# Kernel optimization log

Measured on AMD Instinct MI355X. Metric: run time of the kernel, lower is better.

Reference implementation:

```python
import jax, jax.numpy as jnp
import numpy as np

N, E = 50000, 500000
A, R, EB, EH, H, C, AH, SH, S, AV = 64, 20, 32, 64, 4, 32, 128, 64, 32, 32
EPS = 1e-8
MAX_DIST = 0.5   # nm, maximum_interaction_radius
SCALE = 1.0      # nm, scale_factor


def physnet_rbf(d):
    # PhysNet radial basis: exp(-beta * (exp(-d) - mu_k)^2), mu_k in [exp(-r_cut), 1]
    mu = jnp.linspace(np.exp(-MAX_DIST), 1.0, R).astype(jnp.float32)
    beta = jnp.float32((2.0 / R * (1.0 - np.exp(-MAX_DIST))) ** -2)
    return jnp.exp(-beta * (jnp.exp(-d)[:, None] - mu) ** 2)  # [E, R]


def _forward(h, x, v, idx_i, idx_j, W_edge_in, b_edge_in, W_edge_h, b_edge_h,
             W_edge_out, b_edge_out, W_att, b_att, W_x_mix, W_node1, b_node1,
             W_node2, b_node2, W_post1, b_post1, W_post2, b_post2,
             W_vel1, b_vel1, W_vel2, w_v_mix):
    n = h.shape[0]
    act = jax.nn.silu
    seg_sum = lambda t, idx: jax.ops.segment_sum(t, idx, num_segments=n)

    # geometry
    r_ij = x[idx_j] - x[idx_i]                       # [E,3]
    d_ij = jnp.sqrt(jnp.sum(r_ij * r_ij, -1) + EPS)  # [E]
    dir_ij = r_ij / (d_ij[:, None] + EPS)            # [E,3]

    # update_edge: gather, RBF filter, edge MLP
    h_cat = jnp.concatenate([h[idx_i], h[idx_j]], -1)                 # [E,2A]
    filtered = physnet_rbf(d_ij) * (h_cat @ W_edge_in + b_edge_in)    # [E,R]
    e_in = jnp.concatenate([h_cat, filtered, d_ij[:, None] / SCALE], -1)
    h_ij_edge = act(e_in @ W_edge_h + b_edge_h) @ W_edge_out + b_edge_out  # [E,EB]

    # semantic attention: CELU logits + segment softmax over receivers per head
    logits = jax.nn.celu(h_ij_edge @ W_att + b_att, alpha=2.0)        # [E,H]
    seg_max = jax.ops.segment_max(logits, idx_i, num_segments=n)      # [n,H]
    exp_l = jnp.exp(logits - seg_max[idx_i])
    denom = seg_sum(exp_l, idx_i)
    att = exp_l / (denom[idx_i] + EPS)                                # [E,H]
    h_ij_semantic = (att[:, :, None] * h_ij_edge[:, None, :]).reshape(-1, H * EB)

    # neighborhood aggregation (scatter-add)
    h_i_semantic = seg_sum(h_ij_semantic, idx_i)                      # [n,H*EB]

    # spatial attention
    mix = jnp.tanh(h_ij_semantic @ W_x_mix)                           # [E,C]
    combinations = dir_ij[:, None, :] * mix[:, :, None]               # [E,C,3]
    counts = jnp.maximum(seg_sum(jnp.ones((idx_i.shape[0],), h.dtype), idx_i), 1.0)
    comb_mean = seg_sum(combinations, idx_i) / counts[:, None, None]  # scatter-mean
    comb_norm2 = jnp.sum(comb_mean * comb_mean, -1)                   # [n,C]
    h_i_spatial = act(act(comb_norm2 @ W_post1 + b_post1) @ W_post2 + b_post2)

    # node update (residual)
    node_in = jnp.concatenate([h, h_i_semantic, h_i_spatial], -1)
    h_upd = h + act(act(node_in @ W_node1 + b_node1) @ W_node2 + b_node2)

    # velocity / coordinate update
    v_ij = jnp.einsum('ecx,c->ex', combinations, w_v_mix)             # [E,3]
    dv = seg_sum(v_ij, idx_i) / counts[:, None]                       # scatter-mean
    gate = 2.0 * jax.nn.sigmoid(act(h_upd @ W_vel1 + b_vel1) @ W_vel2)  # [n,1]
    v_upd = gate * v + dv
    x_upd = x + v_upd
    return h_upd, x_upd, v_upd


def _p(k, shape, scale=0.05):
    return jax.random.normal(k, shape, dtype=jnp.float32) * scale


def setup_inputs() -> dict:
    key = jax.random.key(0)
    ks = jax.random.split(key, 24)
    return {
        'h': jax.random.normal(ks[0], (N, A), dtype=jnp.float32),
        'x': jax.random.normal(ks[1], (N, 3), dtype=jnp.float32),
        'v': jax.random.normal(ks[2], (N, 3), dtype=jnp.float32),
        'idx_i': jax.random.randint(ks[3], (E,), 0, N),
        'idx_j': jax.random.randint(ks[4], (E,), 0, N),
        'W_edge_in': _p(ks[5], (2 * A, R)), 'b_edge_in': jnp.zeros((R,), jnp.float32),
        'W_edge_h': _p(ks[6], (2 * A + R + 1, EH)), 'b_edge_h': jnp.zeros((EH,), jnp.float32),
        'W_edge_out': _p(ks[7], (EH, EB)), 'b_edge_out': jnp.zeros((EB,), jnp.float32),
        'W_att': _p(ks[8], (EB, H)), 'b_att': jnp.zeros((H,), jnp.float32),
        'W_x_mix': _p(ks[9], (H * EB, C)),
        'W_node1': _p(ks[10], (A + H * EB + S, AH)), 'b_node1': jnp.zeros((AH,), jnp.float32),
        'W_node2': _p(ks[11], (AH, A)), 'b_node2': jnp.zeros((A,), jnp.float32),
        'W_post1': _p(ks[12], (C, SH)), 'b_post1': jnp.zeros((SH,), jnp.float32),
        'W_post2': _p(ks[13], (SH, S)), 'b_post2': jnp.zeros((S,), jnp.float32),
        'W_vel1': _p(ks[14], (A, AV)), 'b_vel1': jnp.zeros((AV,), jnp.float32),
        'W_vel2': _p(ks[15], (AV, 1)),
        'w_v_mix': _p(ks[16], (C,)),
    }


def reference(h, x, v, idx_i, idx_j, W_edge_in, b_edge_in, W_edge_h, b_edge_h,
              W_edge_out, b_edge_out, W_att, b_att, W_x_mix, W_node1, b_node1,
              W_node2, b_node2, W_post1, b_post1, W_post2, b_post2,
              W_vel1, b_vel1, W_vel2, w_v_mix):
    return _forward(h, x, v, idx_i, idx_j, W_edge_in, b_edge_in, W_edge_h, b_edge_h,
                    W_edge_out, b_edge_out, W_att, b_att, W_x_mix, W_node1, b_node1,
                    W_node2, b_node2, W_post1, b_post1, W_post2, b_post2,
                    W_vel1, b_vel1, W_vel2, w_v_mix)
```

## Files before the change

kernel.cpp:

```cpp
#include <hip/hip_runtime.h>
#include <math.h>

#define DA 64
#define NODEIN_DIM 224
#define EPSC 1e-8f

typedef short v8s __attribute__((ext_vector_type(8)));
typedef float v4f __attribute__((ext_vector_type(4)));
typedef unsigned short ushort_t;

__device__ __forceinline__ float siluf(float v) { return v / (1.0f + __expf(-v)); }

__device__ __forceinline__ void atomAddF(float* p, float v) {
#if defined(__HIP_DEVICE_COMPILE__)
  unsafeAtomicAdd(p, v);
#else
  atomicAdd(p, v);
#endif
}

__device__ __forceinline__ unsigned short f2bfu(float f) {
  union { float f; unsigned u; } v; v.f = f;
  unsigned r = v.u + 0x7fffu + ((v.u >> 16) & 1u);
  return (unsigned short)(r >> 16);
}
__device__ __forceinline__ short f2bfs(float f) { return (short)f2bfu(f); }
__device__ __forceinline__ float bf2f(ushort_t s) {
  union { unsigned u; float f; } v; v.u = ((unsigned)s) << 16; return v.f;
}

#define MU0 0.60653065971263342f
#define DMU ((1.0f - 0.60653065971263342f) / 19.0f)
#define BETA ((float)(1.0 / (0.039346934028736658 * 0.039346934028736658)))

__global__ __launch_bounds__(256) void cast_h(
    const float* __restrict__ hsrc, ushort_t* __restrict__ hb, int n4)
{
  const int i = blockIdx.x * blockDim.x + threadIdx.x;
  if (i < n4) {
    const float4 fv = ((const float4*)hsrc)[i];
    ushort4 o;
    o.x = f2bfu(fv.x); o.y = f2bfu(fv.y); o.z = f2bfu(fv.z); o.w = f2bfu(fv.w);
    ((ushort4*)hb)[i] = o;
  }
}

__global__ __launch_bounds__(256) void deg_count(
    const int* __restrict__ idx_i, int* __restrict__ deg, int E)
{
  const int stride = gridDim.x * blockDim.x;
  for (int e = blockIdx.x * blockDim.x + threadIdx.x; e < E; e += stride)
    atomicAdd(&deg[idx_i[e]], 1);
}

#define SCAN_B 64
#define SCAN_T (SCAN_B * 256)

__global__ __launch_bounds__(256) void deg_tsum(
    const int* __restrict__ deg, int* __restrict__ tsum, int N, int C)
{
  const int g = blockIdx.x * blockDim.x + threadIdx.x;
  const int lo = g * C;
  const int hi = (lo + C < N) ? (lo + C) : N;
  int s = 0;
  for (int i = lo; i < hi; ++i) s += deg[i];
  tsum[g] = s;
}

__global__ __launch_bounds__(256) void scan_tsum(int* __restrict__ tsum)
{
  __shared__ int ps[256];
  const int t = threadIdx.x;
  const int per = SCAN_T / 256;
  const int lo = t * per;
  int s = 0;
  for (int i = 0; i < per; ++i) s += tsum[lo + i];
  ps[t] = s;
  __syncthreads();
  if (t == 0) {
    int a = 0;
    for (int i = 0; i < 256; ++i) { const int v = ps[i]; ps[i] = a; a += v; }
  }
  __syncthreads();
  int acc = ps[t];
  for (int i = 0; i < per; ++i) {
    const int v = tsum[lo + i];
    tsum[lo + i] = acc;
    acc += v;
  }
}

__global__ __launch_bounds__(256) void write_csr(
    const int* __restrict__ deg, const int* __restrict__ tpre,
    int* __restrict__ rowstart, int* __restrict__ cursor,
    float* __restrict__ counts, int N, int C)
{
  const int g = blockIdx.x * blockDim.x + threadIdx.x;
  const int lo = g * C;
  const int hi = (lo + C < N) ? (lo + C) : N;
  int acc = tpre[g];
  for (int i = lo; i < hi; ++i) {
    const int d = deg[i];
    rowstart[i] = acc;
    cursor[i] = acc;
    counts[i] = (float)d;
    acc += d;
  }
  if (hi == N) rowstart[N] = acc;
}

__global__ __launch_bounds__(256) void bucket_edges(
    const int* __restrict__ idx_i, const int* __restrict__ idx_j,
    int* __restrict__ cursor, int* __restrict__ iperm,
    int* __restrict__ jperm, int E)
{
  const int stride = gridDim.x * blockDim.x;
  for (int e = blockIdx.x * blockDim.x + threadIdx.x; e < E; e += stride) {
    const int ii = idx_i[e];
    const int pos = atomicAdd(&cursor[ii], 1);
    iperm[pos] = ii;
    jperm[pos] = idx_j[e];
  }
}

__global__ __launch_bounds__(256) void edge_f1(
    const ushort_t* __restrict__ h_bf, const float* __restrict__ x,
    const int* __restrict__ iperm, const int* __restrict__ jperm,
    const float* __restrict__ W_in, const float* __restrict__ b_in,
    ushort_t* __restrict__ Filt, float* __restrict__ dirb, int E)
{
  const int tid = blockIdx.x * blockDim.x + threadIdx.x;
  const int wid = tid >> 6;
  const int lane = threadIdx.x & 63;
  const int nw = (gridDim.x * blockDim.x) >> 6;
  const int l15 = lane & 15;
  const int q = lane >> 4;

  v8s bfr[4][2];
  #pragma unroll
  for (int kc = 0; kc < 4; ++kc)
    #pragma unroll
    for (int nt = 0; nt < 2; ++nt)
      #pragma unroll
      for (int j = 0; j < 8; ++j) {
        const int k = kc * 32 + q * 8 + j;
        const int col = nt * 16 + l15;
        bfr[kc][nt][j] = (col < 20) ? f2bfs(W_in[k * 20 + col]) : (short)0;
      }
  float bin[2], mu[2];
  #pragma unroll
  for (int nt = 0; nt < 2; ++nt) {
    const int col = nt * 16 + l15;
    bin[nt] = (col < 20) ? b_in[col] : 0.0f;
    mu[nt] = MU0 + (float)col * DMU;
  }

  const int ntiles = (E + 15) >> 4;
  for (int t = wid; t < ntiles; t += nw) {
    const int row = t * 16 + l15;
    const int rowL = (row < E) ? row : (E - 1);
    const int ii = iperm[rowL];
    const int jj = jperm[rowL];

    v8s afr[4];
    afr[0] = *(const v8s*)(h_bf + (size_t)ii * 64 + q * 8);
    afr[1] = *(const v8s*)(h_bf + (size_t)ii * 64 + 32 + q * 8);
    afr[2] = *(const v8s*)(h_bf + (size_t)jj * 64 + q * 8);
    afr[3] = *(const v8s*)(h_bf + (size_t)jj * 64 + 32 + q * 8);

    float dval = 0.0f;
    if (lane < 16 && row < E) {
      const float rx = x[jj * 3 + 0] - x[ii * 3 + 0];
      const float ry = x[jj * 3 + 1] - x[ii * 3 + 1];
      const float rz = x[jj * 3 + 2] - x[ii * 3 + 2];
      const float d = sqrtf(rx * rx + ry * ry + rz * rz + EPSC);
      dval = d;
      const float inv = 1.0f / (d + EPSC);
      dirb[row * 3 + 0] = rx * inv;
      dirb[row * 3 + 1] = ry * inv;
      dirb[row * 3 + 2] = rz * inv;
    }

    v4f acc[2];
    #pragma unroll
    for (int nt = 0; nt < 2; ++nt) {
      v4f a = {0.f, 0.f, 0.f, 0.f};
      #pragma unroll
      for (int kc = 0; kc < 4; ++kc)
        a = __builtin_amdgcn_mfma_f32_16x16x32_bf16(afr[kc], bfr[kc][nt], a, 0, 0, 0);
      acc[nt] = a;
    }

    const int rowb = t * 16 + q * 4;
    float dr[4], edr[4];
    #pragma unroll
    for (int r = 0; r < 4; ++r) {
      dr[r] = __shfl(dval, q * 4 + r);
      edr[r] = __expf(-dr[r]);
    }
    #pragma unroll
    for (int nt = 0; nt < 2; ++nt) {
      const int col = nt * 16 + l15;
      #pragma unroll
      for (int r = 0; r < 4; ++r) {
        ushort_t ov;
        if (col < 20) {
          const float tt = edr[r] - mu[nt];
          ov = f2bfu((acc[nt][r] + bin[nt]) * __expf(-BETA * tt * tt));
        } else if (col == 20) {
          ov = f2bfu(dr[r]);
        } else {
          ov = 0;
        }
        if (rowb + r < E) Filt[(size_t)(rowb + r) * 32 + col] = ov;
      }
    }
  }
}

#define THS 72
__global__ __launch_bounds__(256) void edge_f2(
    const ushort_t* __restrict__ h_bf,
    const int* __restrict__ iperm, const int* __restrict__ jperm,
    const ushort_t* __restrict__ Filt,
    const float* __restrict__ W_h, const float* __restrict__ b_h,
    const float* __restrict__ W_out, const float* __restrict__ b_out,
    const float* __restrict__ W_att, const float* __restrict__ b_att,
    ushort_t* __restrict__ heb, float* __restrict__ expl,
    float* __restrict__ denom, int E)
{
  __shared__ ushort_t sB2[20 * 64 * 8];
  __shared__ ushort_t sB3[4 * 64 * 8];
  __shared__ ushort_t tH[4][16 * THS];

  const int tid = threadIdx.x;
  for (int idx = tid; idx < 20 * 64 * 8; idx += 256) {
    const int j = idx & 7;
    const int ln = (idx >> 3) & 63;
    const int f = idx >> 9;
    const int k = (f >> 2) * 32 + (ln >> 4) * 8 + j;
    const int col = (f & 3) * 16 + (ln & 15);
    sB2[idx] = (k < 149) ? f2bfu(W_h[k * 64 + col]) : (ushort_t)0;
  }
  for (int idx = tid; idx < 4 * 64 * 8; idx += 256) {
    const int j = idx & 7;
    const int ln = (idx >> 3) & 63;
    const int f = idx >> 9;
    const int k = (f >> 1) * 32 + (ln >> 4) * 8 + j;
    const int col = (f & 1) * 16 + (ln & 15);
    sB3[idx] = f2bfu(W_out[k * 32 + col]);
  }
  __syncthreads();

  const int gtid = blockIdx.x * blockDim.x + tid;
  const int wid = gtid >> 6;
  const int lane = tid & 63;
  const int w = tid >> 6;
  const int nw = (gridDim.x * blockDim.x) >> 6;
  const int l15 = lane & 15;
  const int q = lane >> 4;

  const ushort_t* b2l = sB2 + lane * 8;
  const ushort_t* b3l = sB3 + lane * 8;

  float bias2[4];
  #pragma unroll
  for (int nt = 0; nt < 4; ++nt) bias2[nt] = b_h[nt * 16 + l15];
  float bias3[2];
  #pragma unroll
  for (int nt = 0; nt < 2; ++nt) bias3[nt] = b_out[nt * 16 + l15];

  v8s battf;
  #pragma unroll
  for (int j = 0; j < 8; ++j)
    battf[j] = (l15 < 4) ? f2bfs(W_att[(q * 8 + j) * 4 + l15]) : (short)0;
  const float bav = (l15 < 4) ? b_att[l15] : 0.0f;

  const int ntiles = (E + 15) >> 4;

  int iiC = 0;
  v8s afr[5];
  if (wid < ntiles) {
    const int row0 = wid * 16 + l15;
    const int rowL0 = (row0 < E) ? row0 : (E - 1);
    iiC = iperm[rowL0];
    const int jj0 = jperm[rowL0];
    afr[0] = *(const v8s*)(h_bf + (size_t)iiC * 64 + q * 8);
    afr[1] = *(const v8s*)(h_bf + (size_t)iiC * 64 + 32 + q * 8);
    afr[2] = *(const v8s*)(h_bf + (size_t)jj0 * 64 + q * 8);
    afr[3] = *(const v8s*)(h_bf + (size_t)jj0 * 64 + 32 + q * 8);
    afr[4] = *(const v8s*)(Filt + (size_t)rowL0 * 32 + q * 8);
  }

  for (int t = wid; t < ntiles; t += nw) {
    const int tn = t + nw;
    int iiN = 0;
    v8s nfr[5];
    if (tn < ntiles) {
      const int rowN = tn * 16 + l15;
      const int rowLN = (rowN < E) ? rowN : (E - 1);
      iiN = iperm[rowLN];
      const int jjN = jperm[rowLN];
      nfr[0] = *(const v8s*)(h_bf + (size_t)iiN * 64 + q * 8);
      nfr[1] = *(const v8s*)(h_bf + (size_t)iiN * 64 + 32 + q * 8);
      nfr[2] = *(const v8s*)(h_bf + (size_t)jjN * 64 + q * 8);
      nfr[3] = *(const v8s*)(h_bf + (size_t)jjN * 64 + 32 + q * 8);
      nfr[4] = *(const v8s*)(Filt + (size_t)rowLN * 32 + q * 8);
    }

    v4f acc2[4];
    #pragma unroll
    for (int nt = 0; nt < 4; ++nt) {
      v4f a = {0.f, 0.f, 0.f, 0.f};
      #pragma unroll
      for (int kc = 0; kc < 5; ++kc) {
        const v8s bfrag = *(const v8s*)(b2l + (kc * 4 + nt) * 512);
        a = __builtin_amdgcn_mfma_f32_16x16x32_bf16(afr[kc], bfrag, a, 0, 0, 0);
      }
      acc2[nt] = a;
    }

    #pragma unroll
    for (int nt = 0; nt < 4; ++nt) {
      #pragma unroll
      for (int r = 0; r < 4; ++r)
        tH[w][(q * 4 + r) * THS + nt * 16 + l15] =
            f2bfu(siluf(acc2[nt][r] + bias2[nt]));
    }
    __builtin_amdgcn_wave_barrier();

    v8s af3[2];
    af3[0] = *(const v8s*)&tH[w][l15 * THS + q * 8];
    af3[1] = *(const v8s*)&tH[w][l15 * THS + 32 + q * 8];

    v4f acc3[2];
    #pragma unroll
    for (int nt = 0; nt < 2; ++nt) {
      v4f a = {0.f, 0.f, 0.f, 0.f};
      #pragma unroll
      for (int kc = 0; kc < 2; ++kc) {
        const v8s bfrag = *(const v8s*)(b3l + (kc * 2 + nt) * 512);
        a = __builtin_amdgcn_mfma_f32_16x16x32_bf16(af3[kc], bfrag, a, 0, 0, 0);
      }
      acc3[nt] = a;
    }
    __builtin_amdgcn_wave_barrier();

    const int rowb = t * 16 + q * 4;
    #pragma unroll
    for (int nt = 0; nt < 2; ++nt) {
      const int col = nt * 16 + l15;
      #pragma unroll
      for (int r = 0; r < 4; ++r) {
        const ushort_t hv = f2bfu(acc3[nt][r] + bias3[nt]);
        tH[w][(q * 4 + r) * THS + col] = hv;
        if (rowb + r < E) heb[(size_t)(rowb + r) * 32 + col] = hv;
      }
    }
    __builtin_amdgcn_wave_barrier();

    const v8s afA = *(const v8s*)&tH[w][l15 * THS + q * 8];
    v4f az = {0.f, 0.f, 0.f, 0.f};
    const v4f aacc = __builtin_amdgcn_mfma_f32_16x16x32_bf16(afA, battf, az, 0, 0, 0);

    int ii_r[4];
    #pragma unroll
    for (int r = 0; r < 4; ++r) ii_r[r] = __shfl(iiC, q * 4 + r);

    if (l15 < 4) {
      #pragma unroll
      for (int r = 0; r < 4; ++r) {
        if (rowb + r < E) {
          const float la = aacc[r] + bav;
          const float l = (la > 0.f) ? la : 2.0f * (__expf(0.5f * la) - 1.0f);
          const float ev = __expf(l);
          expl[(size_t)(rowb + r) * 4 + l15] = ev;
          atomAddF(&denom[ii_r[r] * 4 + l15], ev);
        }
      }
    }
    __builtin_amdgcn_wave_barrier();

    iiC = iiN;
    afr[0] = nfr[0]; afr[1] = nfr[1]; afr[2] = nfr[2];
    afr[3] = nfr[3]; afr[4] = nfr[4];
  }
}

__global__ __launch_bounds__(256) void mix_kernel(
    const ushort_t* __restrict__ heb, const int* __restrict__ iperm,
    const float* __restrict__ expl, const float* __restrict__ denom,
    const float* __restrict__ W_xmix, const float* __restrict__ w_vmix,
    ushort_t* __restrict__ mixE, float* __restrict__ pE, int E)
{
  const int tid = blockIdx.x * blockDim.x + threadIdx.x;
  const int wid = tid >> 6;
  const int lane = threadIdx.x & 63;
  const int nw = (gridDim.x * blockDim.x) >> 6;
  const int l15 = lane & 15;
  const int q = lane >> 4;

  v8s bfr[4][2];
  #pragma unroll
  for (int kc = 0; kc < 4; ++kc)
    #pragma unroll
    for (int nt = 0; nt < 2; ++nt)
      #pragma unroll
      for (int j = 0; j < 8; ++j) {
        const int k = kc * 32 + q * 8 + j;
        const int col = nt * 16 + l15;
        bfr[kc][nt][j] = f2bfs(W_xmix[k * 32 + col]);
      }
  float wv[2];
  wv[0] = w_vmix[l15];
  wv[1] = w_vmix[16 + l15];

  const int ntiles = (E + 15) >> 4;
  for (int t = wid; t < ntiles; t += nw) {
    const int row = t * 16 + l15;
    const int rowL = (row < E) ? row : (E - 1);
    const int ii = iperm[rowL];
    float att[4];
    #pragma unroll
    for (int hh = 0; hh < 4; ++hh)
      att[hh] = expl[(size_t)rowL * 4 + hh] / (denom[ii * 4 + hh] + EPSC);

    const v8s hech = *(const v8s*)(heb + (size_t)rowL * 32 + q * 8);
    float hef[8];
    #pragma unroll
    for (int j = 0; j < 8; ++j) hef[j] = bf2f((ushort_t)hech[j]);

    v8s afr[4];
    #pragma unroll
    for (int kc = 0; kc < 4; ++kc)
      #pragma unroll
      for (int j = 0; j < 8; ++j)
        afr[kc][j] = f2bfs(att[kc] * hef[j]);

    v4f acc[2];
    #pragma unroll
    for (int nt = 0; nt < 2; ++nt) {
      v4f a = {0.f, 0.f, 0.f, 0.f};
      #pragma unroll
      for (int kc = 0; kc < 4; ++kc)
        a = __builtin_amdgcn_mfma_f32_16x16x32_bf16(afr[kc], bfr[kc][nt], a, 0, 0, 0);
      acc[nt] = a;
    }

    const int rowb = t * 16 + q * 4;
    float pr[4];
    #pragma unroll
    for (int r = 0; r < 4; ++r) {
      const float m0 = tanhf(acc[0][r]);
      const float m1 = tanhf(acc[1][r]);
      if (rowb + r < E) {
        mixE[(size_t)(rowb + r) * 32 + l15] = f2bfu(m0);
        mixE[(size_t)(rowb + r) * 32 + 16 + l15] = f2bfu(m1);
      }
      pr[r] = m0 * wv[0] + m1 * wv[1];
    }
    #pragma unroll
    for (int r = 0; r < 4; ++r) {
      pr[r] += __shfl_xor(pr[r], 1);
      pr[r] += __shfl_xor(pr[r], 2);
      pr[r] += __shfl_xor(pr[r], 4);
      pr[r] += __shfl_xor(pr[r], 8);
      if (l15 == 0 && rowb + r < E) pE[rowb + r] = pr[r];
    }
  }
}

__global__ __launch_bounds__(256) void node_reduce(
    const int* __restrict__ rowstart,
    const ushort_t* __restrict__ heb, const ushort_t* __restrict__ mixE,
    const float* __restrict__ expl, const float* __restrict__ denom,
    const float* __restrict__ dirb, const float* __restrict__ pE,
    ushort_t* __restrict__ hsem, float* __restrict__ comb_sum,
    float* __restrict__ dv_sum, int N)
{
  const int tid = blockIdx.x * blockDim.x + threadIdx.x;
  const int wid = tid >> 6;
  const int lane = threadIdx.x & 63;
  const int nw = (gridDim.x * blockDim.x) >> 6;
  const int hh = lane >> 5;
  const int eb = lane & 31;

  for (int n = wid; n < N; n += nw) {
    const int s = rowstart[n];
    const int epd = rowstart[n + 1];
    float semA = 0.f, semB = 0.f;
    float cx = 0.f, cy = 0.f, cz = 0.f;
    float dvx = 0.f, dvy = 0.f, dvz = 0.f;
    for (int k = s; k < epd; ++k) {
      const float he = bf2f(heb[(size_t)k * 32 + eb]);
      const float ea = expl[(size_t)k * 4 + hh];
      const float ec = expl[(size_t)k * 4 + 2 + hh];
      semA += ea * he;
      semB += ec * he;
      const float dx = dirb[k * 3 + 0];
      const float dy = dirb[k * 3 + 1];
      const float dz = dirb[k * 3 + 2];
      if (lane < 32) {
        const float m = bf2f(mixE[(size_t)k * 32 + lane]);
        cx += dx * m; cy += dy * m; cz += dz * m;
      }
      if (lane == 0) {
        const float pe = pE[k];
        dvx += dx * pe; dvy += dy * pe; dvz += dz * pe;
      }
    }
    const float dA = denom[n * 4 + hh] + EPSC;
    const float dB = denom[n * 4 + 2 + hh] + EPSC;
    hsem[(size_t)n * 128 + lane] = f2bfu(semA / dA);
    hsem[(size_t)n * 128 + 64 + lane] = f2bfu(semB / dB);
    if (lane < 32) {
      comb_sum[(size_t)n * 96 + lane * 3 + 0] = cx;
      comb_sum[(size_t)n * 96 + lane * 3 + 1] = cy;
      comb_sum[(size_t)n * 96 + lane * 3 + 2] = cz;
    }
    if (lane == 0) {
      dv_sum[n * 3 + 0] = dvx;
      dv_sum[n * 3 + 1] = dvy;
      dv_sum[n * 3 + 2] = dvz;
    }
  }
}

#define W1S 232
__global__ __launch_bounds__(256) void node_c1_mfma(
    const ushort_t* __restrict__ h_bf, const ushort_t* __restrict__ hsem,
    const float* __restrict__ comb_sum, const float* __restrict__ counts,
    const float* __restrict__ W_post1, const float* __restrict__ b_post1,
    const float* __restrict__ W_post2, const float* __restrict__ b_post2,
    const float* __restrict__ W_node1, const float* __restrict__ b_node1,
    ushort_t* __restrict__ nh_out, int N)
{
  __shared__ ushort_t sW1t[128 * W1S];
  __shared__ ushort_t tp[4][16 * THS];

  const int tid = threadIdx.x;
  for (int idx = tid; idx < 224 * 128; idx += 256) {
    const int k = idx >> 7;
    const int c = idx & 127;
    sW1t[c * W1S + k] = f2bfu(W_node1[idx]);
  }
  __syncthreads();

  const int lane = tid & 63;
  const int w = tid >> 6;
  const int l15 = lane & 15;
  const int q = lane >> 4;

  v8s bp1[4];
  #pragma unroll
  for (int nt = 0; nt < 4; ++nt)
    #pragma unroll
    for (int j = 0; j < 8; ++j)
      bp1[nt][j] = f2bfs(W_post1[(q * 8 + j) * 64 + nt * 16 + l15]);
  v8s bp2[2][2];
  #pragma unroll
  for (int kc = 0; kc < 2; ++kc)
    #pragma unroll
    for (int nt = 0; nt < 2; ++nt)
      #pragma unroll
      for (int j = 0; j < 8; ++j)
        bp2[kc][nt][j] = f2bfs(W_post2[(kc * 32 + q * 8 + j) * 32 + nt * 16 + l15]);
  float bb1[4];
  #pragma unroll
  for (int nt = 0; nt < 4; ++nt) bb1[nt] = b_post1[nt * 16 + l15];
  float bb2[2];
  #pragma unroll
  for (int nt = 0; nt < 2; ++nt) bb2[nt] = b_post2[nt * 16 + l15];
  float b1[8];
  #pragma unroll
  for (int nt = 0; nt < 8; ++nt) b1[nt] = b_node1[nt * 16 + l15];

  const int gw = blockIdx.x * 4 + w;
  const int nwv = gridDim.x * 4;
  const int ntiles = (N + 15) >> 4;

  for (int t = gw; t < ntiles; t += nwv) {
    const int row = t * 16 + l15;
    const int rowL = (row < N) ? row : (N - 1);

    const float inv = 1.0f / fmaxf(counts[rowL], 1.0f);
    const float4* cs = (const float4*)(comb_sum + (size_t)rowL * 96 + q * 24);
    float cf[24];
    #pragma unroll
    for (int b = 0; b < 6; ++b) {
      const float4 cv = cs[b];
      cf[b * 4 + 0] = cv.x; cf[b * 4 + 1] = cv.y;
      cf[b * 4 + 2] = cv.z; cf[b * 4 + 3] = cv.w;
    }
    v8s a1;
    #pragma unroll
    for (int j = 0; j < 8; ++j) {
      const float vx = cf[j * 3 + 0] * inv;
      const float vy = cf[j * 3 + 1] * inv;
      const float vz = cf[j * 3 + 2] * inv;
      a1[j] = f2bfs(vx * vx + vy * vy + vz * vz);
    }

    v4f p1[4];
    #pragma unroll
    for (int nt = 0; nt < 4; ++nt) {
      v4f a = {0.f, 0.f, 0.f, 0.f};
      p1[nt] = __builtin_amdgcn_mfma_f32_16x16x32_bf16(a1, bp1[nt], a, 0, 0, 0);
    }
    #pragma unroll
    for (int nt = 0; nt < 4; ++nt)
      #pragma unroll
      for (int r = 0; r < 4; ++r)
        tp[w][(q * 4 + r) * THS + nt * 16 + l15] =
            f2bfu(siluf(p1[nt][r] + bb1[nt]));
    __builtin_amdgcn_wave_barrier();

    v8s a2[2];
    a2[0] = *(const v8s*)&tp[w][l15 * THS + q * 8];
    a2[1] = *(const v8s*)&tp[w][l15 * THS + 32 + q * 8];

    v4f p2[2];
    #pragma unroll
    for (int nt = 0; nt < 2; ++nt) {
      v4f a = {0.f, 0.f, 0.f, 0.f};
      #pragma unroll
      for (int kc = 0; kc < 2; ++kc)
        a = __builtin_amdgcn_mfma_f32_16x16x32_bf16(a2[kc], bp2[kc][nt], a, 0, 0, 0);
      p2[nt] = a;
    }
    __builtin_amdgcn_wave_barrier();
    #pragma unroll
    for (int nt = 0; nt < 2; ++nt)
      #pragma unroll
      for (int r = 0; r < 4; ++r)
        tp[w][(q * 4 + r) * THS + nt * 16 + l15] =
            f2bfu(siluf(p2[nt][r] + bb2[nt]));
    __builtin_amdgcn_wave_barrier();

    v8s af[7];
    af[0] = *(const v8s*)(h_bf + (size_t)rowL * 64 + q * 8);
    af[1] = *(const v8s*)(h_bf + (size_t)rowL * 64 + 32 + q * 8);
    #pragma unroll
    for (int kc = 0; kc < 4; ++kc)
      af[2 + kc] = *(const v8s*)(hsem + (size_t)rowL * 128 + kc * 32 + q * 8);
    af[6] = *(const v8s*)&tp[w][l15 * THS + q * 8];

    v4f acc[8];
    #pragma unroll
    for (int nt = 0; nt < 8; ++nt) acc[nt] = (v4f){0.f, 0.f, 0.f, 0.f};
    #pragma unroll
    for (int kc = 0; kc < 7; ++kc) {
      #pragma unroll
      for (int nt = 0; nt < 8; ++nt) {
        const v8s bfrag =
            *(const v8s*)&sW1t[(nt * 16 + l15) * W1S + kc * 32 + q * 8];
        acc[nt] = __builtin_amdgcn_mfma_f32_16x16x32_bf16(af[kc], bfrag, acc[nt], 0, 0, 0);
      }
    }

    const int rowb = t * 16 + q * 4;
    #pragma unroll
    for (int nt = 0; nt < 8; ++nt) {
      #pragma unroll
      for (int r = 0; r < 4; ++r)
        if (rowb + r < N)
          nh_out[(size_t)(rowb + r) * 128 + nt * 16 + l15] =
              f2bfu(siluf(acc[nt][r] + b1[nt]));
    }
  }
}

__global__ __launch_bounds__(256) void node_c2_mfma(
    const float* __restrict__ h, const float* __restrict__ x,
    const float* __restrict__ v, const ushort_t* __restrict__ nh,
    const float* __restrict__ dv_sum, const float* __restrict__ counts,
    const float* __restrict__ W_node2, const float* __restrict__ b_node2,
    const float* __restrict__ W_vel1, const float* __restrict__ b_vel1,
    const float* __restrict__ W_vel2,
    float* __restrict__ out, int N)
{
  __shared__ ushort_t sW2[16 * 64 * 8];
  __shared__ ushort_t sWv[4 * 64 * 8];
  __shared__ ushort_t tH[4][16 * THS];
  __shared__ float sg[4][16];

  const int tid = threadIdx.x;
  for (int idx = tid; idx < 16 * 64 * 8; idx += 256) {
    const int j = idx & 7;
    const int ln = (idx >> 3) & 63;
    const int f = idx >> 9;
    const int k = (f >> 2) * 32 + (ln >> 4) * 8 + j;
    const int col = (f & 3) * 16 + (ln & 15);
    sW2[idx] = f2bfu(W_node2[k * 64 + col]);
  }
  for (int idx = tid; idx < 4 * 64 * 8; idx += 256) {
    const int j = idx & 7;
    const int ln = (idx >> 3) & 63;
    const int f = idx >> 9;
    const int k = (f >> 1) * 32 + (ln >> 4) * 8 + j;
    const int col = (f & 1) * 16 + (ln & 15);
    sWv[idx] = f2bfu(W_vel1[k * 32 + col]);
  }
  __syncthreads();

  const int lane = tid & 63;
  const int w = tid >> 6;
  const int l15 = lane & 15;
  const int q = lane >> 4;

  const ushort_t* w2l = sW2 + lane * 8;
  const ushort_t* wvl = sWv + lane * 8;

  float b2[4];
  #pragma unroll
  for (int nt = 0; nt < 4; ++nt) b2[nt] = b_node2[nt * 16 + l15];
  float bv[2];
  #pragma unroll
  for (int nt = 0; nt < 2; ++nt) bv[nt] = b_vel1[nt * 16 + l15];
  float wv2[2];
  #pragma unroll
  for (int nt = 0; nt < 2; ++nt) wv2[nt] = W_vel2[nt * 16 + l15];

  const int gw = blockIdx.x * 4 + w;
  const int nwv = gridDim.x * 4;
  const int ntiles = (N + 15) >> 4;

  for (int t = gw; t < ntiles; t += nwv) {
    const int row = t * 16 + l15;
    const int rowL = (row < N) ? row : (N - 1);

    v8s af[4];
    #pragma unroll
    for (int kc = 0; kc < 4; ++kc)
      af[kc] = *(const v8s*)(nh + (size_t)rowL * 128 + kc * 32 + q * 8);

    v4f acc[4];
    #pragma unroll
    for (int nt = 0; nt < 4; ++nt) {
      v4f a = {0.f, 0.f, 0.f, 0.f};
      #pragma unroll
      for (int kc = 0; kc < 4; ++kc) {
        const v8s bfrag = *(const v8s*)(w2l + (kc * 4 + nt) * 512);
        a = __builtin_amdgcn_mfma_f32_16x16x32_bf16(af[kc], bfrag, a, 0, 0, 0);
      }
      acc[nt] = a;
    }

    const int rowb = t * 16 + q * 4;
    #pragma unroll
    for (int nt = 0; nt < 4; ++nt) {
      const int col = nt * 16 + l15;
      #pragma unroll
      for (int r = 0; r < 4; ++r) {
        const int n = rowb + r;
        if (n < N) {
          const float hu = h[(size_t)n * 64 + col] + siluf(acc[nt][r] + b2[nt]);
          out[(size_t)n * 64 + col] = hu;
          tH[w][(q * 4 + r) * THS + col] = f2bfu(hu);
        }
      }
    }
    __builtin_amdgcn_wave_barrier();

    v8s a2[2];
    a2[0] = *(const v8s*)&tH[w][l15 * THS + q * 8];
    a2[1] = *(const v8s*)&tH[w][l15 * THS + 32 + q * 8];
    v4f av[2];
    #pragma unroll
    for (int nt = 0; nt < 2; ++nt) {
      v4f a = {0.f, 0.f, 0.f, 0.f};
      #pragma unroll
      for (int kc = 0; kc < 2; ++kc) {
        const v8s bfrag = *(const v8s*)(wvl + (kc * 2 + nt) * 512);
        a = __builtin_amdgcn_mfma_f32_16x16x32_bf16(a2[kc], bfrag, a, 0, 0, 0);
      }
      av[nt] = a;
    }

    #pragma unroll
    for (int r = 0; r < 4; ++r) {
      float pr = siluf(av[0][r] + bv[0]) * wv2[0] +
                 siluf(av[1][r] + bv[1]) * wv2[1];
      pr += __shfl_xor(pr, 1);
      pr += __shfl_xor(pr, 2);
      pr += __shfl_xor(pr, 4);
      pr += __shfl_xor(pr, 8);
      if (l15 == 0) sg[w][q * 4 + r] = 2.0f / (1.0f + __expf(-pr));
    }
    __builtin_amdgcn_wave_barrier();

    if (lane < 48) {
      const int rr = lane / 3;
      const int c = lane % 3;
      const int n = t * 16 + rr;
      if (n < N) {
        const float gate = sg[w][rr];
        const float cnt = fmaxf(counts[n], 1.0f);
        const float dv = dv_sum[n * 3 + c] / cnt;
        const float vu = gate * v[n * 3 + c] + dv;
        out[(size_t)N * 64 + (size_t)n * 3 + c] = x[n * 3 + c] + vu;
        out[(size_t)N * 64 + (size_t)N * 3 + (size_t)n * 3 + c] = vu;
      }
    }
    __builtin_amdgcn_wave_barrier();
  }
}

extern "C" void kernel_launch(void* const* d_in, const int* in_sizes, int n_in,
                              void* d_out, int out_size, void* d_ws, size_t ws_size,
                              hipStream_t stream) {
  const float* h   = (const float*)d_in[0];
  const float* x   = (const float*)d_in[1];
  const float* v   = (const float*)d_in[2];
  const int* idx_i = (const int*)d_in[3];
  const int* idx_j = (const int*)d_in[4];
  const float* W_edge_in  = (const float*)d_in[5];
  const float* b_edge_in  = (const float*)d_in[6];
  const float* W_edge_h   = (const float*)d_in[7];
  const float* b_edge_h   = (const float*)d_in[8];
  const float* W_edge_out = (const float*)d_in[9];
  const float* b_edge_out = (const float*)d_in[10];
  const float* W_att      = (const float*)d_in[11];
  const float* b_att      = (const float*)d_in[12];
  const float* W_x_mix    = (const float*)d_in[13];
  const float* W_node1    = (const float*)d_in[14];
  const float* b_node1    = (const float*)d_in[15];
  const float* W_node2    = (const float*)d_in[16];
  const float* b_node2    = (const float*)d_in[17];
  const float* W_post1    = (const float*)d_in[18];
  const float* b_post1    = (const float*)d_in[19];
  const float* W_post2    = (const float*)d_in[20];
  const float* b_post2    = (const float*)d_in[21];
  const float* W_vel1     = (const float*)d_in[22];
  const float* b_vel1     = (const float*)d_in[23];
  const float* W_vel2     = (const float*)d_in[24];
  const float* w_v_mix    = (const float*)d_in[25];

  const int E = in_sizes[3];
  const int N = in_sizes[0] / DA;

  float* ws = (float*)d_ws;
  size_t off = 0;
  float* denom    = ws + off; off += (size_t)N * 4;
  int*   deg      = (int*)(ws + off); off += (size_t)N;
  const size_t zeroBytes = off * sizeof(float);
  float* counts   = ws + off; off += (size_t)N;
  int*   rowstart = (int*)(ws + off); off += (size_t)N + 4;
  int*   cursor   = (int*)(ws + off); off += (size_t)N;
  int*   tsum     = (int*)(ws + off); off += (size_t)SCAN_T;
  int*   iperm    = (int*)(ws + off); off += (size_t)E;
  int*   jperm    = (int*)(ws + off); off += (size_t)E;
  float* pE       = ws + off; off += (size_t)E;
  float* expl     = ws + off; off += (size_t)E * 4;
  float* dirb     = ws + off; off += (size_t)E * 3;
  float* hsemR    = ws + off; off += (size_t)N * 64;
  float* comb_sum = ws + off; off += (size_t)N * 96;
  float* dv_sum   = ws + off; off += (size_t)N * 4;
  float* hbfR     = ws + off; off += (size_t)N * 32;
  float* fltR     = ws + off; off += (size_t)E * 16;
  float* hebR     = ws + off; off += (size_t)E * 16;

  ushort_t* h_bf = (ushort_t*)hbfR;
  ushort_t* hsem = (ushort_t*)hsemR;
  ushort_t* Filt = (ushort_t*)fltR;
  ushort_t* heb  = (ushort_t*)hebR;
  ushort_t* mixE = (ushort_t*)fltR;
  ushort_t* nh   = (ushort_t*)fltR;

  hipMemsetAsync(d_ws, 0, zeroBytes, stream);

  {
    const int n4 = (N * 64) / 4;
    cast_h<<<(n4 + 255) / 256, 256, 0, stream>>>(h, h_bf, n4);
  }
  deg_count<<<512, 256, 0, stream>>>(idx_i, deg, E);
  {
    const int C = (N + SCAN_T - 1) / SCAN_T;
    deg_tsum<<<SCAN_B, 256, 0, stream>>>(deg, tsum, N, C);
    scan_tsum<<<1, 256, 0, stream>>>(tsum);
    write_csr<<<SCAN_B, 256, 0, stream>>>(deg, tsum, rowstart, cursor, counts, N, C);
  }
  bucket_edges<<<512, 256, 0, stream>>>(idx_i, idx_j, cursor, iperm, jperm, E);
  edge_f1<<<1024, 256, 0, stream>>>(h_bf, x, iperm, jperm, W_edge_in,
                                    b_edge_in, Filt, dirb, E);
  edge_f2<<<1024, 256, 0, stream>>>(h_bf, iperm, jperm, Filt, W_edge_h,
                                    b_edge_h, W_edge_out, b_edge_out,
                                    W_att, b_att, heb, expl, denom, E);
  mix_kernel<<<1024, 256, 0, stream>>>(heb, iperm, expl, denom, W_x_mix,
                                       w_v_mix, mixE, pE, E);
  node_reduce<<<2048, 256, 0, stream>>>(rowstart, heb, mixE, expl, denom,
                                        dirb, pE, hsem, comb_sum, dv_sum, N);
  node_c1_mfma<<<512, 256, 0, stream>>>(
      h_bf, hsem, comb_sum, counts, W_post1, b_post1, W_post2, b_post2,
      W_node1, b_node1, nh, N);
  node_c2_mfma<<<512, 256, 0, stream>>>(
      h, x, v, nh, dv_sum, counts, W_node2, b_node2, W_vel1, b_vel1, W_vel2,
      (float*)d_out, N);
}
```

Baseline: 410.0 us.

## Fuse edge filter and edge MLP kernels, unroll node_reduce edge loop

Merges the RBF-filter kernel into the edge MLP kernel so the filtered features go through per-wave shared memory instead of a global Filt buffer, and reuses the gathered h fragments for both matmuls. This removes one kernel launch, the global write and re-read of Filt, and the duplicate gathers of h. The fused kernel uses more LDS (an extra W_in tile), which may lower occupancy. Separately, the per-node reduction loop is unrolled by four so more loads are in flight at once.

```diff
diff --git a/kernel.cpp b/kernel.cpp
--- a/kernel.cpp
+++ b/kernel.cpp
@@ -123,118 +123,32 @@
   }
 }
 
-__global__ __launch_bounds__(256) void edge_f1(
+#define THS 72
+__global__ __launch_bounds__(256) void edge_f12(
     const ushort_t* __restrict__ h_bf, const float* __restrict__ x,
     const int* __restrict__ iperm, const int* __restrict__ jperm,
     const float* __restrict__ W_in, const float* __restrict__ b_in,
-    ushort_t* __restrict__ Filt, float* __restrict__ dirb, int E)
-{
-  const int tid = blockIdx.x * blockDim.x + threadIdx.x;
-  const int wid = tid >> 6;
-  const int lane = threadIdx.x & 63;
-  const int nw = (gridDim.x * blockDim.x) >> 6;
-  const int l15 = lane & 15;
-  const int q = lane >> 4;
-
-  v8s bfr[4][2];
-  #pragma unroll
-  for (int kc = 0; kc < 4; ++kc)
-    #pragma unroll
-    for (int nt = 0; nt < 2; ++nt)
-      #pragma unroll
-      for (int j = 0; j < 8; ++j) {
-        const int k = kc * 32 + q * 8 + j;
-        const int col = nt * 16 + l15;
-        bfr[kc][nt][j] = (col < 20) ? f2bfs(W_in[k * 20 + col]) : (short)0;
-      }
-  float bin[2], mu[2];
-  #pragma unroll
-  for (int nt = 0; nt < 2; ++nt) {
-    const int col = nt * 16 + l15;
-    bin[nt] = (col < 20) ? b_in[col] : 0.0f;
-    mu[nt] = MU0 + (float)col * DMU;
-  }
-
-  const int ntiles = (E + 15) >> 4;
-  for (int t = wid; t < ntiles; t += nw) {
-    const int row = t * 16 + l15;
-    const int rowL = (row < E) ? row : (E - 1);
-    const int ii = iperm[rowL];
-    const int jj = jperm[rowL];
-
-    v8s afr[4];
-    afr[0] = *(const v8s*)(h_bf + (size_t)ii * 64 + q * 8);
-    afr[1] = *(const v8s*)(h_bf + (size_t)ii * 64 + 32 + q * 8);
-    afr[2] = *(const v8s*)(h_bf + (size_t)jj * 64 + q * 8);
-    afr[3] = *(const v8s*)(h_bf + (size_t)jj * 64 + 32 + q * 8);
-
-    float dval = 0.0f;
-    if (lane < 16 && row < E) {
-      const float rx = x[jj * 3 + 0] - x[ii * 3 + 0];
-      const float ry = x[jj * 3 + 1] - x[ii * 3 + 1];
-      const float rz = x[jj * 3 + 2] - x[ii * 3 + 2];
-      const float d = sqrtf(rx * rx + ry * ry + rz * rz + EPSC);
-      dval = d;
-      const float inv = 1.0f / (d + EPSC);
-      dirb[row * 3 + 0] = rx * inv;
-      dirb[row * 3 + 1] = ry * inv;
-      dirb[row * 3 + 2] = rz * inv;
-    }
-
-    v4f acc[2];
-    #pragma unroll
-    for (int nt = 0; nt < 2; ++nt) {
-      v4f a = {0.f, 0.f, 0.f, 0.f};
-      #pragma unroll
-      for (int kc = 0; kc < 4; ++kc)
-        a = __builtin_amdgcn_mfma_f32_16x16x32_bf16(afr[kc], bfr[kc][nt], a, 0, 0, 0);
-      acc[nt] = a;
-    }
-
-    const int rowb = t * 16 + q * 4;
-    float dr[4], edr[4];
-    #pragma unroll
-    for (int r = 0; r < 4; ++r) {
-      dr[r] = __shfl(dval, q * 4 + r);
-      edr[r] = __expf(-dr[r]);
-    }
-    #pragma unroll
-    for (int nt = 0; nt < 2; ++nt) {
-      const int col = nt * 16 + l15;
-      #pragma unroll
-      for (int r = 0; r < 4; ++r) {
-        ushort_t ov;
-        if (col < 20) {
-          const float tt = edr[r] - mu[nt];
-          ov = f2bfu((acc[nt][r] + bin[nt]) * __expf(-BETA * tt * tt));
-        } else if (col == 20) {
-          ov = f2bfu(dr[r]);
-        } else {
-          ov = 0;
-        }
-        if (rowb + r < E) Filt[(size_t)(rowb + r) * 32 + col] = ov;
-      }
-    }
-  }
-}
-
-#define THS 72
-__global__ __launch_bounds__(256) void edge_f2(
-    const ushort_t* __restrict__ h_bf,
-    const int* __restrict__ iperm, const int* __restrict__ jperm,
-    const ushort_t* __restrict__ Filt,
     const float* __restrict__ W_h, const float* __restrict__ b_h,
     const float* __restrict__ W_out, const float* __restrict__ b_out,
     const float* __restrict__ W_att, const float* __restrict__ b_att,
-    ushort_t* __restrict__ heb, float* __restrict__ expl,
-    float* __restrict__ denom, int E)
-{
-  __shared__ ushort_t sB2[20 * 64 * 8];
-  __shared__ ushort_t sB3[4 * 64 * 8];
+    float* __restrict__ dirb, ushort_t* __restrict__ heb,
+    float* __restrict__ expl, float* __restrict__ denom, int E)
+{
+  __shared__ ushort_t sB1[8 * 512];
+  __shared__ ushort_t sB2[20 * 512];
+  __shared__ ushort_t sB3[4 * 512];
   __shared__ ushort_t tH[4][16 * THS];
 
   const int tid = threadIdx.x;
-  for (int idx = tid; idx < 20 * 64 * 8; idx += 256) {
+  for (int idx = tid; idx < 8 * 512; idx += 256) {
+    const int j = idx & 7;
+    const int ln = (idx >> 3) & 63;
+    const int f = idx >> 9;
+    const int k = (f >> 1) * 32 + (ln >> 4) * 8 + j;
+    const int col = (f & 1) * 16 + (ln & 15);
+    sB1[idx] = (col < 20) ? f2bfu(W_in[k * 20 + col]) : (ushort_t)0;
+  }
+  for (int idx = tid; idx < 20 * 512; idx += 256) {
     const int j = idx & 7;
     const int ln = (idx >> 3) & 63;
     const int f = idx >> 9;
@@ -242,7 +156,7 @@
     const int col = (f & 3) * 16 + (ln & 15);
     sB2[idx] = (k < 149) ? f2bfu(W_h[k * 64 + col]) : (ushort_t)0;
   }
-  for (int idx = tid; idx < 4 * 64 * 8; idx += 256) {
+  for (int idx = tid; idx < 4 * 512; idx += 256) {
     const int j = idx & 7;
     const int ln = (idx >> 3) & 63;
     const int f = idx >> 9;
@@ -260,9 +174,17 @@
   const int l15 = lane & 15;
   const int q = lane >> 4;
 
+  const ushort_t* b1l = sB1 + lane * 8;
   const ushort_t* b2l = sB2 + lane * 8;
   const ushort_t* b3l = sB3 + lane * 8;
 
+  float bin[2], mu[2];
+  #pragma unroll
+  for (int nt = 0; nt < 2; ++nt) {
+    const int col = nt * 16 + l15;
+    bin[nt] = (col < 20) ? b_in[col] : 0.0f;
+    mu[nt] = MU0 + (float)col * DMU;
+  }
   float bias2[4];
   #pragma unroll
   for (int nt = 0; nt < 4; ++nt) bias2[nt] = b_h[nt * 16 + l15];
@@ -278,45 +200,99 @@
 
   const int ntiles = (E + 15) >> 4;
 
-  int iiC = 0;
-  v8s afr[5];
+  int iiC = 0, jjC = 0;
+  v8s afr[4];
   if (wid < ntiles) {
     const int row0 = wid * 16 + l15;
     const int rowL0 = (row0 < E) ? row0 : (E - 1);
     iiC = iperm[rowL0];
-    const int jj0 = jperm[rowL0];
+    jjC = jperm[rowL0];
     afr[0] = *(const v8s*)(h_bf + (size_t)iiC * 64 + q * 8);
     afr[1] = *(const v8s*)(h_bf + (size_t)iiC * 64 + 32 + q * 8);
-    afr[2] = *(const v8s*)(h_bf + (size_t)jj0 * 64 + q * 8);
-    afr[3] = *(const v8s*)(h_bf + (size_t)jj0 * 64 + 32 + q * 8);
-    afr[4] = *(const v8s*)(Filt + (size_t)rowL0 * 32 + q * 8);
+    afr[2] = *(const v8s*)(h_bf + (size_t)jjC * 64 + q * 8);
+    afr[3] = *(const v8s*)(h_bf + (size_t)jjC * 64 + 32 + q * 8);
   }
 
   for (int t = wid; t < ntiles; t += nw) {
     const int tn = t + nw;
-    int iiN = 0;
-    v8s nfr[5];
+    int iiN = 0, jjN = 0;
+    v8s nfr[4];
     if (tn < ntiles) {
       const int rowN = tn * 16 + l15;
       const int rowLN = (rowN < E) ? rowN : (E - 1);
       iiN = iperm[rowLN];
-      const int jjN = jperm[rowLN];
+      jjN = jperm[rowLN];
       nfr[0] = *(const v8s*)(h_bf + (size_t)iiN * 64 + q * 8);
       nfr[1] = *(const v8s*)(h_bf + (size_t)iiN * 64 + 32 + q * 8);
       nfr[2] = *(const v8s*)(h_bf + (size_t)jjN * 64 + q * 8);
       nfr[3] = *(const v8s*)(h_bf + (size_t)jjN * 64 + 32 + q * 8);
-      nfr[4] = *(const v8s*)(Filt + (size_t)rowLN * 32 + q * 8);
-    }
+    }
+
+    const int row = t * 16 + l15;
+    float dval = 0.0f;
+    if (lane < 16 && row < E) {
+      const float rx = x[jjC * 3 + 0] - x[iiC * 3 + 0];
+      const float ry = x[jjC * 3 + 1] - x[iiC * 3 + 1];
+      const float rz = x[jjC * 3 + 2] - x[iiC * 3 + 2];
+      const float d = sqrtf(rx * rx + ry * ry + rz * rz + EPSC);
+      dval = d;
+      const float inv = 1.0f / (d + EPSC);
+      dirb[row * 3 + 0] = rx * inv;
+      dirb[row * 3 + 1] = ry * inv;
+      dirb[row * 3 + 2] = rz * inv;
+    }
+
+    v4f acc1[2];
+    #pragma unroll
+    for (int nt = 0; nt < 2; ++nt) {
+      v4f a = {0.f, 0.f, 0.f, 0.f};
+      #pragma unroll
+      for (int kc = 0; kc < 4; ++kc) {
+        const v8s bfrag = *(const v8s*)(b1l + (kc * 2 + nt) * 512);
+        a = __builtin_amdgcn_mfma_f32_16x16x32_bf16(afr[kc], bfrag, a, 0, 0, 0);
+      }
+      acc1[nt] = a;
+    }
+
+    float dr[4], edr[4];
+    #pragma unroll
+    for (int r = 0; r < 4; ++r) {
+      dr[r] = __shfl(dval, q * 4 + r);
+      edr[r] = __expf(-dr[r]);
+    }
+    #pragma unroll
+    for (int nt = 0; nt < 2; ++nt) {
+      const int col = nt * 16 + l15;
+      #pragma unroll
+      for (int r = 0; r < 4; ++r) {
+        ushort_t ov;
+        if (col < 20) {
+          const float tt = edr[r] - mu[nt];
+          ov = f2bfu((acc1[nt][r] + bin[nt]) * __expf(-BETA * tt * tt));
+        } else if (col == 20) {
+          ov = f2bfu(dr[r]);
+        } else {
+          ov = 0;
+        }
+        tH[w][(q * 4 + r) * THS + col] = ov;
+      }
+    }
+    __builtin_amdgcn_wave_barrier();
+
+    const v8s afr4 = *(const v8s*)&tH[w][l15 * THS + q * 8];
+    __builtin_amdgcn_wave_barrier();
 
     v4f acc2[4];
     #pragma unroll
     for (int nt = 0; nt < 4; ++nt) {
       v4f a = {0.f, 0.f, 0.f, 0.f};
       #pragma unroll
-      for (int kc = 0; kc < 5; ++kc) {
+      for (int kc = 0; kc < 4; ++kc) {
         const v8s bfrag = *(const v8s*)(b2l + (kc * 4 + nt) * 512);
         a = __builtin_amdgcn_mfma_f32_16x16x32_bf16(afr[kc], bfrag, a, 0, 0, 0);
       }
+      const v8s bfrag4 = *(const v8s*)(b2l + (4 * 4 + nt) * 512);
+      a = __builtin_amdgcn_mfma_f32_16x16x32_bf16(afr4, bfrag4, a, 0, 0, 0);
       acc2[nt] = a;
     }
 
@@ -381,9 +357,8 @@
     }
     __builtin_amdgcn_wave_barrier();
 
-    iiC = iiN;
-    afr[0] = nfr[0]; afr[1] = nfr[1]; afr[2] = nfr[2];
-    afr[3] = nfr[3]; afr[4] = nfr[4];
+    iiC = iiN; jjC = jjN;
+    afr[0] = nfr[0]; afr[1] = nfr[1]; afr[2] = nfr[2]; afr[3] = nfr[3];
   }
 }
 
@@ -491,7 +466,41 @@
     float semA = 0.f, semB = 0.f;
     float cx = 0.f, cy = 0.f, cz = 0.f;
     float dvx = 0.f, dvy = 0.f, dvz = 0.f;
-    for (int k = s; k < epd; ++k) {
+    int k = s;
+    const int e4 = s + ((epd - s) & ~3);
+    for (; k < e4; k += 4) {
+      float he[4], ea[4], ec[4], dx[4], dy[4], dz[4], m[4], pe[4];
+      #pragma unroll
+      for (int u = 0; u < 4; ++u) {
+        he[u] = bf2f(heb[(size_t)(k + u) * 32 + eb]);
+        ea[u] = expl[(size_t)(k + u) * 4 + hh];
+        ec[u] = expl[(size_t)(k + u) * 4 + 2 + hh];
+        dx[u] = dirb[(k + u) * 3 + 0];
+        dy[u] = dirb[(k + u) * 3 + 1];
+        dz[u] = dirb[(k + u) * 3 + 2];
+      }
+      if (lane < 32) {
+        #pragma unroll
+        for (int u = 0; u < 4; ++u)
+          m[u] = bf2f(mixE[(size_t)(k + u) * 32 + lane]);
+      }
+      if (lane == 0) {
+        #pragma unroll
+        for (int u = 0; u < 4; ++u) pe[u] = pE[k + u];
+      }
+      #pragma unroll
+      for (int u = 0; u < 4; ++u) {
+        semA += ea[u] * he[u];
+        semB += ec[u] * he[u];
+        if (lane < 32) {
+          cx += dx[u] * m[u]; cy += dy[u] * m[u]; cz += dz[u] * m[u];
+        }
+        if (lane == 0) {
+          dvx += dx[u] * pe[u]; dvy += dy[u] * pe[u]; dvz += dz[u] * pe[u];
+        }
+      }
+    }
+    for (; k < epd; ++k) {
       const float he = bf2f(heb[(size_t)k * 32 + eb]);
       const float ea = expl[(size_t)k * 4 + hh];
       const float ec = expl[(size_t)k * 4 + 2 + hh];
@@ -862,7 +871,6 @@
 
   ushort_t* h_bf = (ushort_t*)hbfR;
   ushort_t* hsem = (ushort_t*)hsemR;
-  ushort_t* Filt = (ushort_t*)fltR;
   ushort_t* heb  = (ushort_t*)hebR;
   ushort_t* mixE = (ushort_t*)fltR;
   ushort_t* nh   = (ushort_t*)fltR;
@@ -881,11 +889,10 @@
     write_csr<<<SCAN_B, 256, 0, stream>>>(deg, tsum, rowstart, cursor, counts, N, C);
   }
   bucket_edges<<<512, 256, 0, stream>>>(idx_i, idx_j, cursor, iperm, jperm, E);
-  edge_f1<<<1024, 256, 0, stream>>>(h_bf, x, iperm, jperm, W_edge_in,
-                                    b_edge_in, Filt, dirb, E);
-  edge_f2<<<1024, 256, 0, stream>>>(h_bf, iperm, jperm, Filt, W_edge_h,
-                                    b_edge_h, W_edge_out, b_edge_out,
-                                    W_att, b_att, heb, expl, denom, E);
+  edge_f12<<<1024, 256, 0, stream>>>(h_bf, x, iperm, jperm,
+                                     W_edge_in, b_edge_in, W_edge_h, b_edge_h,
+                                     W_edge_out, b_edge_out, W_att, b_att,
+                                     dirb, heb, expl, denom, E);
   mix_kernel<<<1024, 256, 0, stream>>>(heb, iperm, expl, denom, W_x_mix,
                                        w_v_mix, mixE, pE, E);
   node_reduce<<<2048, 256, 0, stream>>>(rowstart, heb, mixE, expl, denom,
```

Measured after the change: 406.2 us. No clear change (-0.9%).
